# Kernel optimization log

Hardware: AMD Instinct MI355X
Metric: run time of the kernel (lower is better)

Reference implementation:

```python
import jax, jax.numpy as jnp
import numpy as np

NEG_SLOPE = 0.2  # keras 'leaky_relu' default negative slope

def _leaky_relu(t):
    return jnp.where(t >= 0, t, NEG_SLOPE * t)

def setup_inputs() -> dict:
    key = jax.random.key(0)
    kx, kq, kk, kv, ko, kg = jax.random.split(key, 6)
    B, H, W, C, A = 4, 64, 64, 256, 128
    x = jax.random.normal(kx, (B, H, W, C), dtype=jnp.float32)
    # 1x1 conv kernels == [Cin, Cout] matrices; glorot-normal-ish scaling
    Wq = jax.random.normal(kq, (C, A), dtype=jnp.float32) * (2.0 / (C + A)) ** 0.5
    Wk = jax.random.normal(kk, (C, A), dtype=jnp.float32) * (2.0 / (C + A)) ** 0.5
    Wv = jax.random.normal(kv, (C, A), dtype=jnp.float32) * (2.0 / (C + A)) ** 0.5
    Wo = jax.random.normal(ko, (A, C), dtype=jnp.float32) * (2.0 / (A + C)) ** 0.5
    # ChannelLearnableMultiplier weight: truncated_normal(0, 0.01) ~ small values near 0
    w_gamma = jax.random.normal(kg, (1, 1, 1, C), dtype=jnp.float32) * 0.01
    return {"x": x, "Wq": Wq, "Wk": Wk, "Wv": Wv, "Wo": Wo, "w_gamma": w_gamma}

def reference(x, Wq, Wk, Wv, Wo, w_gamma):
    B, H, W, C = x.shape
    A = Wq.shape[1]
    # 1x1 conv projections with leaky_relu activation, flatten spatial -> [B, N, A]
    q = _leaky_relu(jnp.einsum('bhwc,ca->bhwa', x, Wq)).reshape(B, H * W, A)
    k = _leaky_relu(jnp.einsum('bhwc,ca->bhwa', x, Wk)).reshape(B, H * W, A)
    v = _leaky_relu(jnp.einsum('bhwc,ca->bhwa', x, Wv)).reshape(B, H * W, A)
    # keras Attention(use_scale=False, score_mode='dot'): softmax(q k^T) v
    scores = jnp.einsum('bnd,bmd->bnm', q, k)          # [B, N, N]
    attn = jax.nn.softmax(scores, axis=-1)
    o = jnp.einsum('bnm,bmd->bnd', attn, v)            # [B, N, A]
    o = o.reshape(B, H, W, A)
    # output 1x1 conv, linear activation
    y = jnp.einsum('bhwa,ac->bhwc', o, Wo)
    # ChannelLearnableMultiplier: tanh(relu(1 + w)) * y
    return jnp.tanh(jax.nn.relu(1.0 + w_gamma)) * y
```

## Files before the change

kernel.cpp:

```cpp
#include <hip/hip_runtime.h>
#include <hip/hip_bf16.h>
#include <cstdint>
#include <cstddef>

typedef __bf16 bf16x8 __attribute__((ext_vector_type(8)));
typedef _Float16 f16x8 __attribute__((ext_vector_type(8)));
typedef short short8 __attribute__((ext_vector_type(8)));
typedef short short4v __attribute__((ext_vector_type(4)));
typedef float f32x4 __attribute__((ext_vector_type(4)));

#if defined(__HIP_DEVICE_COMPILE__)
  #define MFMA16BF(a,b,c)  __builtin_amdgcn_mfma_f32_16x16x16bf16_1k((a),(b),(c),0,0,0)
  #define MFMA32F16(a,b,c) __builtin_amdgcn_mfma_f32_16x16x32_f16((a),(b),(c),0,0,0)
  #define MFMA32BF(a,b,c)  __builtin_amdgcn_mfma_f32_16x16x32_bf16((a),(b),(c),0,0,0)
#else
  #define MFMA16BF(a,b,c)  (c)
  #define MFMA32F16(a,b,c) (c)
  #define MFMA32BF(a,b,c)  (c)
#endif

#if defined(__HIP_DEVICE_COMPILE__) && __has_builtin(__builtin_amdgcn_exp2f)
  #define EXP2F(x) __builtin_amdgcn_exp2f(x)
#else
  #define EXP2F(x) exp2f(x)
#endif

__device__ __forceinline__ void barrier_lds_only() {
    asm volatile("s_waitcnt lgkmcnt(0)\n\ts_barrier" ::: "memory");
}

__device__ __forceinline__ unsigned short f2bf(float f) {
    union { float f; uint32_t u; } v; v.f = f;
    uint32_t u = v.u;
    return (unsigned short)((u + 0x7FFFu + ((u >> 16) & 1u)) >> 16);
}
__device__ __forceinline__ float bf2f(unsigned short h) {
    union { uint32_t u; float f; } v; v.u = ((uint32_t)h) << 16;
    return v.f;
}
__device__ __forceinline__ unsigned short f2h(float f) {
    union { _Float16 h; unsigned short u; } v; v.h = (_Float16)f;
    return v.u;
}

__global__ __launch_bounds__(256) void qkv_kernel(
    const float* __restrict__ x,
    const float* __restrict__ Wq,
    const float* __restrict__ Wk,
    const float* __restrict__ Wv,
    unsigned short* __restrict__ qkv_ws)
{
    const int rowtile = blockIdx.x;
    const int proj    = blockIdx.y;
    const float* W = (proj == 0) ? Wq : ((proj == 1) ? Wk : Wv);
    unsigned short* outqk = qkv_ws + (size_t)proj * 2097152u;
    unsigned short* vt    = qkv_ws + (size_t)2 * 2097152u;
    const bool need_lo = (proj < 2);

    const int tid  = threadIdx.x;
    const int lane = tid & 63, wave = tid >> 6;
    const int lo   = lane & 15, quad = lane >> 4;

    __shared__ __align__(16) unsigned short Xh[64][72], Xl[64][72];
    __shared__ __align__(16) unsigned short Wh[128][72], Wl[128][72];

    f32x4 acc[8];
    #pragma unroll
    for (int i = 0; i < 8; ++i) acc[i] = (f32x4){0.f, 0.f, 0.f, 0.f};

    for (int kc = 0; kc < 4; ++kc) {
        __syncthreads();
        #pragma unroll
        for (int i = 0; i < 4; ++i) {
            int flat4 = (i * 256 + tid) * 4;
            int row = flat4 >> 6, col = flat4 & 63;
            float4 tv4 = *(const float4*)(x + (size_t)(rowtile * 64 + row) * 256 + kc * 64 + col);
            float tv[4] = {tv4.x, tv4.y, tv4.z, tv4.w};
            short4v h, l;
            #pragma unroll
            for (int j = 0; j < 4; ++j) {
                unsigned short hj = f2bf(tv[j]);
                h[j] = (short)hj;
                l[j] = (short)f2bf(tv[j] - bf2f(hj));
            }
            *(short4v*)(&Xh[row][col]) = h;
            if (need_lo) *(short4v*)(&Xl[row][col]) = l;
        }
        {
            int n = tid & 127;
            for (int g = (tid >> 7); g < 16; g += 2) {
                int k0 = g * 4;
                short4v h, l;
                #pragma unroll
                for (int j = 0; j < 4; ++j) {
                    float wv = W[(size_t)(kc * 64 + k0 + j) * 128 + n];
                    unsigned short hj = f2bf(wv);
                    h[j] = (short)hj;
                    l[j] = (short)f2bf(wv - bf2f(hj));
                }
                *(short4v*)(&Wh[n][k0]) = h;
                if (need_lo) *(short4v*)(&Wl[n][k0]) = l;
            }
        }
        __syncthreads();
        #pragma unroll
        for (int ks = 0; ks < 2; ++ks) {
            bf16x8 ah = *(const bf16x8*)(&Xh[wave * 16 + lo][ks * 32 + quad * 8]);
            #pragma unroll
            for (int nb = 0; nb < 8; ++nb) {
                bf16x8 bh = *(const bf16x8*)(&Wh[nb * 16 + lo][ks * 32 + quad * 8]);
                acc[nb] = MFMA32BF(ah, bh, acc[nb]);
                if (need_lo) {
                    bf16x8 al = *(const bf16x8*)(&Xl[wave * 16 + lo][ks * 32 + quad * 8]);
                    bf16x8 bl = *(const bf16x8*)(&Wl[nb * 16 + lo][ks * 32 + quad * 8]);
                    acc[nb] = MFMA32BF(al, bh, acc[nb]);
                    acc[nb] = MFMA32BF(ah, bl, acc[nb]);
                }
            }
        }
    }
    if (proj < 2) {
        #pragma unroll
        for (int nb = 0; nb < 8; ++nb) {
            #pragma unroll
            for (int r = 0; r < 4; ++r) {
                float v = acc[nb][r];
                v = (v >= 0.f) ? v : 0.2f * v;
                int m = rowtile * 64 + wave * 16 + quad * 4 + r;
                outqk[(size_t)m * 128 + nb * 16 + lo] = f2h(v);
            }
        }
    } else {
        const int b  = rowtile >> 6;
        const int sb = (rowtile & 63) * 64;
        #pragma unroll
        for (int nb = 0; nb < 8; ++nb) {
            #pragma unroll
            for (int r = 0; r < 4; ++r) {
                float v = acc[nb][r];
                v = (v >= 0.f) ? v : 0.2f * v;
                int seq = sb + wave * 16 + quad * 4 + r;
                int d   = nb * 16 + lo;
                vt[(size_t)b * 524288 + (size_t)d * 4096 + seq] = f2bf(v);
            }
        }
    }
}

__global__ __launch_bounds__(256) void attn_kernel(
    const unsigned short* __restrict__ qkv_ws,
    unsigned short* __restrict__ part,
    float* __restrict__ lpart,
    int chunk)
{
    const int b  = blockIdx.x;
    const int qt = blockIdx.y;
    const int z  = blockIdx.z;
    const int tid  = threadIdx.x;
    const int lane = tid & 63, wave = tid >> 6;
    const int lo   = lane & 15, quad = lane >> 4;

    const unsigned short* q  = qkv_ws;
    const unsigned short* k  = qkv_ws + 2097152u;
    const unsigned short* vt = qkv_ws + (size_t)2 * 2097152u + (size_t)b * 524288u;

    __shared__ __align__(16) unsigned short Ks[2][32][136];
    __shared__ __align__(16) unsigned short Vt[2][128][40];

    const int qbase = qt * 128 + wave * 32;
    f16x8 qf[2][4];
    #pragma unroll
    for (int g = 0; g < 2; ++g)
        #pragma unroll
        for (int ks = 0; ks < 4; ++ks)
            qf[g][ks] = *(const f16x8*)(q + ((size_t)(b * 4096 + qbase + g * 16 + lo)) * 128
                                          + ks * 32 + quad * 8);

    f32x4 oacc[2][8];
    #pragma unroll
    for (int g = 0; g < 2; ++g)
        #pragma unroll
        for (int i = 0; i < 8; ++i) oacc[g][i] = (f32x4){0.f, 0.f, 0.f, 0.f};
    float Lsum[2] = {1e-30f, 1e-30f};

    const float LOG2E  = 1.44269504088896f;
    const float NSHIFT = -40.0f * 1.44269504088896f;

    const int krow0 = tid >> 4, kcol0 = (tid & 15) * 8;
    const int krow1 = 16 + (tid >> 4);
    const int vd = tid >> 2, vc = tid & 3;
    const int vst  = vc >> 1;
    const int colA = ((2 * vc) & 3) * 8 + vst * 4;
    const int colB = ((2 * vc + 1) & 3) * 8 + vst * 4;

    const int niter = chunk >> 5;
    const int sbase = z * chunk;

    short8 ka, kb, va, vb;
    ka = *(const short8*)(k + ((size_t)(b * 4096 + sbase + krow0)) * 128 + kcol0);
    kb = *(const short8*)(k + ((size_t)(b * 4096 + sbase + krow1)) * 128 + kcol0);
    va = *(const short8*)(vt + (size_t)vd * 4096 + sbase + vc * 8);
    vb = *(const short8*)(vt + (size_t)(vd + 64) * 4096 + sbase + vc * 8);
    *(short8*)(&Ks[0][krow0][kcol0]) = ka;
    *(short8*)(&Ks[0][krow1][kcol0]) = kb;
    {
        short4v a0 = {va[0], va[1], va[2], va[3]}, a1 = {va[4], va[5], va[6], va[7]};
        short4v b0 = {vb[0], vb[1], vb[2], vb[3]}, b1 = {vb[4], vb[5], vb[6], vb[7]};
        *(short4v*)(&Vt[0][vd][colA])      = a0;
        *(short4v*)(&Vt[0][vd][colB])      = a1;
        *(short4v*)(&Vt[0][vd + 64][colA]) = b0;
        *(short4v*)(&Vt[0][vd + 64][colB]) = b1;
    }
    if (1 < niter) {
        const int s1 = sbase + 32;
        ka = *(const short8*)(k + ((size_t)(b * 4096 + s1 + krow0)) * 128 + kcol0);
        kb = *(const short8*)(k + ((size_t)(b * 4096 + s1 + krow1)) * 128 + kcol0);
        va = *(const short8*)(vt + (size_t)vd * 4096 + s1 + vc * 8);
        vb = *(const short8*)(vt + (size_t)(vd + 64) * 4096 + s1 + vc * 8);
    }
    barrier_lds_only();

    short4v Pp[2][2];

    for (int kt = 0; kt < niter; ++kt) {
        const int cur = kt & 1, oth = cur ^ 1;

        f32x4 sT[2][2];
        sT[0][0] = (f32x4){0.f,0.f,0.f,0.f}; sT[0][1] = (f32x4){0.f,0.f,0.f,0.f};
        sT[1][0] = (f32x4){0.f,0.f,0.f,0.f}; sT[1][1] = (f32x4){0.f,0.f,0.f,0.f};
        #pragma unroll
        for (int ks = 0; ks < 4; ++ks) {
            #pragma unroll
            for (int st = 0; st < 2; ++st) {
                f16x8 kf = *(const f16x8*)(&Ks[cur][st * 16 + lo][ks * 32 + quad * 8]);
                sT[0][st] = MFMA32F16(kf, qf[0][ks], sT[0][st]);
                sT[1][st] = MFMA32F16(kf, qf[1][ks], sT[1][st]);
            }
        }
        if (kt > 0) {
            #pragma unroll
            for (int nb = 0; nb < 8; ++nb) {
                short8 vv = *(const short8*)(&Vt[oth][nb * 16 + lo][quad * 8]);
                short4v v0 = {vv[0], vv[1], vv[2], vv[3]};
                short4v v1 = {vv[4], vv[5], vv[6], vv[7]};
                #pragma unroll
                for (int g = 0; g < 2; ++g) {
                    oacc[g][nb] = MFMA16BF(Pp[g][0], v0, oacc[g][nb]);
                    oacc[g][nb] = MFMA16BF(Pp[g][1], v1, oacc[g][nb]);
                }
            }
        }
        barrier_lds_only();
        if (kt + 1 < niter) {
            *(short8*)(&Ks[oth][krow0][kcol0]) = ka;
            *(short8*)(&Ks[oth][krow1][kcol0]) = kb;
            short4v a0 = {va[0], va[1], va[2], va[3]}, a1 = {va[4], va[5], va[6], va[7]};
            short4v b0 = {vb[0], vb[1], vb[2], vb[3]}, b1 = {vb[4], vb[5], vb[6], vb[7]};
            *(short4v*)(&Vt[oth][vd][colA])      = a0;
            *(short4v*)(&Vt[oth][vd][colB])      = a1;
            *(short4v*)(&Vt[oth][vd + 64][colA]) = b0;
            *(short4v*)(&Vt[oth][vd + 64][colB]) = b1;
        }
        if (kt + 2 < niter) {
            const int s2 = sbase + (kt + 2) * 32;
            ka = *(const short8*)(k + ((size_t)(b * 4096 + s2 + krow0)) * 128 + kcol0);
            kb = *(const short8*)(k + ((size_t)(b * 4096 + s2 + krow1)) * 128 + kcol0);
            va = *(const short8*)(vt + (size_t)vd * 4096 + s2 + vc * 8);
            vb = *(const short8*)(vt + (size_t)(vd + 64) * 4096 + s2 + vc * 8);
        }
        #pragma unroll
        for (int g = 0; g < 2; ++g) {
            #pragma unroll
            for (int st = 0; st < 2; ++st) {
                #pragma unroll
                for (int r = 0; r < 4; ++r) {
                    float t = fminf(fmaf(sT[g][st][r], LOG2E, NSHIFT), 125.0f);
                    union { float f; uint32_t u; } pv; pv.f = EXP2F(t);
                    unsigned short pt = (unsigned short)(pv.u >> 16);
                    Lsum[g] += bf2f(pt);
                    Pp[g][st][r] = (short)pt;
                }
            }
        }
        barrier_lds_only();
    }
    {
        const int last = (niter - 1) & 1;
        #pragma unroll
        for (int nb = 0; nb < 8; ++nb) {
            short8 vv = *(const short8*)(&Vt[last][nb * 16 + lo][quad * 8]);
            short4v v0 = {vv[0], vv[1], vv[2], vv[3]};
            short4v v1 = {vv[4], vv[5], vv[6], vv[7]};
            #pragma unroll
            for (int g = 0; g < 2; ++g) {
                oacc[g][nb] = MFMA16BF(Pp[g][0], v0, oacc[g][nb]);
                oacc[g][nb] = MFMA16BF(Pp[g][1], v1, oacc[g][nb]);
            }
        }
    }

    #pragma unroll
    for (int g = 0; g < 2; ++g) {
        float xr = Lsum[g];
        xr += __shfl_xor(xr, 16, 64);
        xr += __shfl_xor(xr, 32, 64);
        Lsum[g] = xr;
    }
    #pragma unroll
    for (int g = 0; g < 2; ++g) {
        #pragma unroll
        for (int nb = 0; nb < 8; ++nb) {
            #pragma unroll
            for (int r = 0; r < 4; ++r) {
                int m = b * 4096 + qbase + g * 16 + quad * 4 + r;
                part[((size_t)z * 16384 + m) * 128 + nb * 16 + lo] = f2bf(oacc[g][nb][r]);
            }
        }
        if (lane < 16) {
            int m = b * 4096 + qbase + g * 16 + lane;
            lpart[(size_t)z * 16384 + m] = Lsum[g];
        }
    }
}

__global__ __launch_bounds__(256) void outproj_kernel(
    const unsigned short* __restrict__ part,
    const float* __restrict__ lpart,
    const float* __restrict__ Wo,
    const float* __restrict__ wg,
    float* __restrict__ out,
    int nsplit)
{
    const int rowtile = blockIdx.x;
    const int tid  = threadIdx.x;
    const int lane = tid & 63, wave = tid >> 6;
    const int lo   = lane & 15, quad = lane >> 4;

    __shared__ __align__(16) unsigned short Os[32][136];
    __shared__ __align__(16) unsigned short WoT[128][136];
    __shared__ float gl[256];

    {
        float g = 1.0f + wg[tid];
        if (g < 0.f) g = 0.f;
        gl[tid] = tanhf(g);
    }
    #pragma unroll
    for (int i = 0; i < 2; ++i) {
        int flat = (i * 256 + tid) * 8;
        int row = flat >> 7, col = flat & 127;
        int m = rowtile * 32 + row;
        float acc8[8] = {0.f,0.f,0.f,0.f,0.f,0.f,0.f,0.f};
        float l = 0.f;
        for (int zz = 0; zz < nsplit; ++zz) {
            short8 t = *(const short8*)(part + ((size_t)zz * 16384 + m) * 128 + col);
            #pragma unroll
            for (int j = 0; j < 8; ++j) acc8[j] += bf2f((unsigned short)t[j]);
            l += lpart[(size_t)zz * 16384 + m];
        }
        float inv = 1.0f / l;
        short8 o8;
        #pragma unroll
        for (int j = 0; j < 8; ++j) o8[j] = (short)f2bf(acc8[j] * inv);
        *(short8*)(&Os[row][col]) = o8;
    }

    const int rg = wave & 1, csub = wave >> 1;

    for (int ch = 0; ch < 2; ++ch) {
        if (ch) __syncthreads();
        {
            int c = tid & 127;
            for (int g = (tid >> 7); g < 16; g += 2) {
                int a0 = g * 8;
                short8 t;
                #pragma unroll
                for (int j = 0; j < 8; ++j)
                    t[j] = (short)f2bf(Wo[(size_t)(a0 + j) * 256 + ch * 128 + c]);
                *(short8*)(&WoT[c][a0]) = t;
            }
        }
        __syncthreads();

        f32x4 acc[4];
        #pragma unroll
        for (int i = 0; i < 4; ++i) acc[i] = (f32x4){0.f, 0.f, 0.f, 0.f};
        #pragma unroll
        for (int ks = 0; ks < 4; ++ks) {
            bf16x8 a = *(const bf16x8*)(&Os[rg * 16 + lo][ks * 32 + quad * 8]);
            #pragma unroll
            for (int nb = 0; nb < 4; ++nb) {
                bf16x8 bf = *(const bf16x8*)(&WoT[csub * 64 + nb * 16 + lo][ks * 32 + quad * 8]);
                acc[nb] = MFMA32BF(a, bf, acc[nb]);
            }
        }
        #pragma unroll
        for (int nb = 0; nb < 4; ++nb) {
            int c = ch * 128 + csub * 64 + nb * 16 + lo;
            float g = gl[c];
            #pragma unroll
            for (int r = 0; r < 4; ++r) {
                int m = rowtile * 32 + rg * 16 + quad * 4 + r;
                out[(size_t)m * 256 + c] = acc[nb][r] * g;
            }
        }
    }
}

extern "C" void kernel_launch(void* const* d_in, const int* in_sizes, int n_in,
                              void* d_out, int out_size, void* d_ws, size_t ws_size,
                              hipStream_t stream) {
    const float* x  = (const float*)d_in[0];
    const float* Wq = (const float*)d_in[1];
    const float* Wk = (const float*)d_in[2];
    const float* Wv = (const float*)d_in[3];
    const float* Wo = (const float*)d_in[4];
    const float* wg = (const float*)d_in[5];
    float* out = (float*)d_out;

    unsigned short* ws = (unsigned short*)d_ws;
    const int nsplit = (ws_size >= (size_t)47000000) ? 8 : 4;
    const int chunk  = 4096 / nsplit;

    unsigned short* qkv_ws = ws;
    unsigned short* part   = ws + (size_t)3 * 2097152u;
    float* lpart = (float*)(part + (size_t)nsplit * 2097152u);

    qkv_kernel<<<dim3(256, 3), 256, 0, stream>>>(x, Wq, Wk, Wv, qkv_ws);
    attn_kernel<<<dim3(4, 32, nsplit), 256, 0, stream>>>(qkv_ws, part, lpart, chunk);
    outproj_kernel<<<dim3(512), 256, 0, stream>>>(part, lpart, Wo, wg, out, nsplit);
}
```

Measured before the change: 180.3 us.

## Pre-split weights into MFMA fragment layout and fuse QKV projections per tile

Adds a small prep kernel that converts Wq/Wk/Wv once into bf16 hi/lo pairs in MFMA fragment order, transposes Wo to bf16, and computes the gamma multiplier. The QKV kernel then handles all three projections in one block per row tile, reading weight fragments straight from global memory, and double-buffers the x tile in LDS with register prefetch. Together these avoid converting the same weights in every block and converting x three times. The cost is an extra launch, more accumulator registers (three sets of eight) that may lower occupancy, and weight fragments read from global or L2 on each k-step instead of from LDS. The prep buffers reuse the partial-output workspace region, which is safe only because attention overwrites it after qkv has finished reading.

```diff
diff --git a/kernel.cpp b/kernel.cpp
--- a/kernel.cpp
+++ b/kernel.cpp
@@ -43,101 +43,176 @@
     return v.u;
 }
 
+__global__ __launch_bounds__(256) void prep_kernel(
+    const float* __restrict__ Wq, const float* __restrict__ Wk,
+    const float* __restrict__ Wv, const float* __restrict__ Wo,
+    const float* __restrict__ wg,
+    unsigned short* __restrict__ wfh,
+    unsigned short* __restrict__ wfl,
+    unsigned short* __restrict__ wot,
+    float* __restrict__ gamma)
+{
+    const int bid = blockIdx.x, t = threadIdx.x;
+    __shared__ __align__(16) unsigned short Tsc[64][136];
+    if (bid < 12) {
+        const int proj = bid >> 2, kc = bid & 3;
+        const float* W = (proj == 0) ? Wq : ((proj == 1) ? Wk : Wv);
+        #pragma unroll
+        for (int s = 0; s < 4; ++s) {
+            int idx = s * 256 + t;
+            int frag = idx >> 6, lane = idx & 63;
+            int ks = frag >> 3, nb = frag & 7;
+            int lo = lane & 15, quad = lane >> 4;
+            short8 h8, l8;
+            #pragma unroll
+            for (int j = 0; j < 8; ++j) {
+                float w = W[(size_t)(kc * 64 + ks * 32 + quad * 8 + j) * 128 + nb * 16 + lo];
+                unsigned short hi = f2bf(w);
+                h8[j] = (short)hi;
+                l8[j] = (short)f2bf(w - bf2f(hi));
+            }
+            size_t base = ((size_t)(proj * 4 + kc) * 16 + frag) * 512 + lane * 8;
+            *(short8*)(wfh + base) = h8;
+            if (proj < 2)
+                *(short8*)(wfl + base) = l8;
+        }
+    } else if (bid < 16) {
+        const int c0 = (bid - 12) * 64;
+        for (int r = 0; r < 32; ++r) {
+            int idx = r * 256 + t;
+            int a = idx >> 6, cc = idx & 63;
+            Tsc[cc][a] = f2bf(Wo[(size_t)a * 256 + c0 + cc]);
+        }
+        __syncthreads();
+        int cc = t >> 2, a0 = (t & 3) * 32;
+        #pragma unroll
+        for (int j = 0; j < 4; ++j)
+            *(short8*)(wot + (size_t)(c0 + cc) * 128 + a0 + j * 8) =
+                *(const short8*)(&Tsc[cc][a0 + j * 8]);
+    } else {
+        float g = 1.0f + wg[t];
+        if (g < 0.f) g = 0.f;
+        gamma[t] = tanhf(g);
+    }
+}
+
 __global__ __launch_bounds__(256) void qkv_kernel(
     const float* __restrict__ x,
-    const float* __restrict__ Wq,
-    const float* __restrict__ Wk,
-    const float* __restrict__ Wv,
+    const unsigned short* __restrict__ wfh,
+    const unsigned short* __restrict__ wfl,
     unsigned short* __restrict__ qkv_ws)
 {
     const int rowtile = blockIdx.x;
-    const int proj    = blockIdx.y;
-    const float* W = (proj == 0) ? Wq : ((proj == 1) ? Wk : Wv);
-    unsigned short* outqk = qkv_ws + (size_t)proj * 2097152u;
-    unsigned short* vt    = qkv_ws + (size_t)2 * 2097152u;
-    const bool need_lo = (proj < 2);
-
     const int tid  = threadIdx.x;
     const int lane = tid & 63, wave = tid >> 6;
     const int lo   = lane & 15, quad = lane >> 4;
 
-    __shared__ __align__(16) unsigned short Xh[64][72], Xl[64][72];
-    __shared__ __align__(16) unsigned short Wh[128][72], Wl[128][72];
-
-    f32x4 acc[8];
-    #pragma unroll
-    for (int i = 0; i < 8; ++i) acc[i] = (f32x4){0.f, 0.f, 0.f, 0.f};
+    __shared__ __align__(16) unsigned short Xh[2][64][72], Xl[2][64][72];
+
+    f32x4 acc[3][8];
+    #pragma unroll
+    for (int p = 0; p < 3; ++p)
+        #pragma unroll
+        for (int i = 0; i < 8; ++i) acc[p][i] = (f32x4){0.f, 0.f, 0.f, 0.f};
+
+    int xrow[4], xcol[4];
+    #pragma unroll
+    for (int i = 0; i < 4; ++i) {
+        int flat4 = (i * 256 + tid) * 4;
+        xrow[i] = flat4 >> 6;
+        xcol[i] = flat4 & 63;
+    }
+    const float* xb = x + (size_t)rowtile * 64 * 256;
+
+    #pragma unroll
+    for (int i = 0; i < 4; ++i) {
+        float4 tv4 = *(const float4*)(xb + (size_t)xrow[i] * 256 + 0 * 64 + xcol[i]);
+        float tv[4] = {tv4.x, tv4.y, tv4.z, tv4.w};
+        short4v h, l;
+        #pragma unroll
+        for (int j = 0; j < 4; ++j) {
+            unsigned short hj = f2bf(tv[j]);
+            h[j] = (short)hj;
+            l[j] = (short)f2bf(tv[j] - bf2f(hj));
+        }
+        *(short4v*)(&Xh[0][xrow[i]][xcol[i]]) = h;
+        *(short4v*)(&Xl[0][xrow[i]][xcol[i]]) = l;
+    }
+    float4 xr[4];
+    #pragma unroll
+    for (int i = 0; i < 4; ++i)
+        xr[i] = *(const float4*)(xb + (size_t)xrow[i] * 256 + 1 * 64 + xcol[i]);
+    barrier_lds_only();
 
     for (int kc = 0; kc < 4; ++kc) {
-        __syncthreads();
-        #pragma unroll
-        for (int i = 0; i < 4; ++i) {
-            int flat4 = (i * 256 + tid) * 4;
-            int row = flat4 >> 6, col = flat4 & 63;
-            float4 tv4 = *(const float4*)(x + (size_t)(rowtile * 64 + row) * 256 + kc * 64 + col);
-            float tv[4] = {tv4.x, tv4.y, tv4.z, tv4.w};
-            short4v h, l;
-            #pragma unroll
-            for (int j = 0; j < 4; ++j) {
-                unsigned short hj = f2bf(tv[j]);
-                h[j] = (short)hj;
-                l[j] = (short)f2bf(tv[j] - bf2f(hj));
-            }
-            *(short4v*)(&Xh[row][col]) = h;
-            if (need_lo) *(short4v*)(&Xl[row][col]) = l;
-        }
-        {
-            int n = tid & 127;
-            for (int g = (tid >> 7); g < 16; g += 2) {
-                int k0 = g * 4;
+        const int cur = kc & 1, oth = cur ^ 1;
+        #pragma unroll
+        for (int proj = 0; proj < 3; ++proj) {
+            const unsigned short* wh = wfh + ((size_t)(proj * 4 + kc) * 16) * 512 + lane * 8;
+            const unsigned short* wl = wfl + ((size_t)(proj * 4 + kc) * 16) * 512 + lane * 8;
+            #pragma unroll
+            for (int ks = 0; ks < 2; ++ks) {
+                bf16x8 ah = *(const bf16x8*)(&Xh[cur][wave * 16 + lo][ks * 32 + quad * 8]);
+                bf16x8 al = *(const bf16x8*)(&Xl[cur][wave * 16 + lo][ks * 32 + quad * 8]);
+                #pragma unroll
+                for (int nb = 0; nb < 8; ++nb) {
+                    bf16x8 bh = *(const bf16x8*)(wh + (size_t)(ks * 8 + nb) * 512);
+                    acc[proj][nb] = MFMA32BF(ah, bh, acc[proj][nb]);
+                    if (proj < 2) {
+                        bf16x8 bl = *(const bf16x8*)(wl + (size_t)(ks * 8 + nb) * 512);
+                        acc[proj][nb] = MFMA32BF(al, bh, acc[proj][nb]);
+                        acc[proj][nb] = MFMA32BF(ah, bl, acc[proj][nb]);
+                    }
+                }
+            }
+        }
+        barrier_lds_only();
+        if (kc + 1 < 4) {
+            #pragma unroll
+            for (int i = 0; i < 4; ++i) {
+                float tv[4] = {xr[i].x, xr[i].y, xr[i].z, xr[i].w};
                 short4v h, l;
                 #pragma unroll
                 for (int j = 0; j < 4; ++j) {
-                    float wv = W[(size_t)(kc * 64 + k0 + j) * 128 + n];
-                    unsigned short hj = f2bf(wv);
+                    unsigned short hj = f2bf(tv[j]);
                     h[j] = (short)hj;
-                    l[j] = (short)f2bf(wv - bf2f(hj));
+                    l[j] = (short)f2bf(tv[j] - bf2f(hj));
                 }
-                *(short4v*)(&Wh[n][k0]) = h;
-                if (need_lo) *(short4v*)(&Wl[n][k0]) = l;
-            }
-        }
-        __syncthreads();
-        #pragma unroll
-        for (int ks = 0; ks < 2; ++ks) {
-            bf16x8 ah = *(const bf16x8*)(&Xh[wave * 16 + lo][ks * 32 + quad * 8]);
-            #pragma unroll
-            for (int nb = 0; nb < 8; ++nb) {
-                bf16x8 bh = *(const bf16x8*)(&Wh[nb * 16 + lo][ks * 32 + quad * 8]);
-                acc[nb] = MFMA32BF(ah, bh, acc[nb]);
-                if (need_lo) {
-                    bf16x8 al = *(const bf16x8*)(&Xl[wave * 16 + lo][ks * 32 + quad * 8]);
-                    bf16x8 bl = *(const bf16x8*)(&Wl[nb * 16 + lo][ks * 32 + quad * 8]);
-                    acc[nb] = MFMA32BF(al, bh, acc[nb]);
-                    acc[nb] = MFMA32BF(ah, bl, acc[nb]);
-                }
-            }
-        }
-    }
-    if (proj < 2) {
+                *(short4v*)(&Xh[oth][xrow[i]][xcol[i]]) = h;
+                *(short4v*)(&Xl[oth][xrow[i]][xcol[i]]) = l;
+            }
+        }
+        if (kc + 2 < 4) {
+            #pragma unroll
+            for (int i = 0; i < 4; ++i)
+                xr[i] = *(const float4*)(xb + (size_t)xrow[i] * 256 + (kc + 2) * 64 + xcol[i]);
+        }
+        barrier_lds_only();
+    }
+
+    #pragma unroll
+    for (int p = 0; p < 2; ++p) {
+        unsigned short* outqk = qkv_ws + (size_t)p * 2097152u;
         #pragma unroll
         for (int nb = 0; nb < 8; ++nb) {
             #pragma unroll
             for (int r = 0; r < 4; ++r) {
-                float v = acc[nb][r];
+                float v = acc[p][nb][r];
                 v = (v >= 0.f) ? v : 0.2f * v;
                 int m = rowtile * 64 + wave * 16 + quad * 4 + r;
                 outqk[(size_t)m * 128 + nb * 16 + lo] = f2h(v);
             }
         }
-    } else {
+    }
+    {
+        unsigned short* vt = qkv_ws + (size_t)2 * 2097152u;
         const int b  = rowtile >> 6;
         const int sb = (rowtile & 63) * 64;
         #pragma unroll
         for (int nb = 0; nb < 8; ++nb) {
             #pragma unroll
             for (int r = 0; r < 4; ++r) {
-                float v = acc[nb][r];
+                float v = acc[2][nb][r];
                 v = (v >= 0.f) ? v : 0.2f * v;
                 int seq = sb + wave * 16 + quad * 4 + r;
                 int d   = nb * 16 + lo;
@@ -326,8 +401,8 @@
 __global__ __launch_bounds__(256) void outproj_kernel(
     const unsigned short* __restrict__ part,
     const float* __restrict__ lpart,
-    const float* __restrict__ Wo,
-    const float* __restrict__ wg,
+    const unsigned short* __restrict__ wot,
+    const float* __restrict__ gamma,
     float* __restrict__ out,
     int nsplit)
 {
@@ -338,13 +413,7 @@
 
     __shared__ __align__(16) unsigned short Os[32][136];
     __shared__ __align__(16) unsigned short WoT[128][136];
-    __shared__ float gl[256];
-
-    {
-        float g = 1.0f + wg[tid];
-        if (g < 0.f) g = 0.f;
-        gl[tid] = tanhf(g);
-    }
+
     #pragma unroll
     for (int i = 0; i < 2; ++i) {
         int flat = (i * 256 + tid) * 8;
@@ -366,20 +435,14 @@
     }
 
     const int rg = wave & 1, csub = wave >> 1;
+    const int wc = tid >> 1, wa0 = (tid & 1) * 64;
 
     for (int ch = 0; ch < 2; ++ch) {
         if (ch) __syncthreads();
-        {
-            int c = tid & 127;
-            for (int g = (tid >> 7); g < 16; g += 2) {
-                int a0 = g * 8;
-                short8 t;
-                #pragma unroll
-                for (int j = 0; j < 8; ++j)
-                    t[j] = (short)f2bf(Wo[(size_t)(a0 + j) * 256 + ch * 128 + c]);
-                *(short8*)(&WoT[c][a0]) = t;
-            }
-        }
+        #pragma unroll
+        for (int j = 0; j < 8; ++j)
+            *(short8*)(&WoT[wc][wa0 + j * 8]) =
+                *(const short8*)(wot + (size_t)(ch * 128 + wc) * 128 + wa0 + j * 8);
         __syncthreads();
 
         f32x4 acc[4];
@@ -397,7 +460,7 @@
         #pragma unroll
         for (int nb = 0; nb < 4; ++nb) {
             int c = ch * 128 + csub * 64 + nb * 16 + lo;
-            float g = gl[c];
+            float g = gamma[c];
             #pragma unroll
             for (int r = 0; r < 4; ++r) {
                 int m = rowtile * 32 + rg * 16 + quad * 4 + r;
@@ -424,9 +487,14 @@
 
     unsigned short* qkv_ws = ws;
     unsigned short* part   = ws + (size_t)3 * 2097152u;
+    unsigned short* wfh    = part;
+    unsigned short* wfl    = part + 98304u;
     float* lpart = (float*)(part + (size_t)nsplit * 2097152u);
-
-    qkv_kernel<<<dim3(256, 3), 256, 0, stream>>>(x, Wq, Wk, Wv, qkv_ws);
+    unsigned short* wot = (unsigned short*)(lpart + (size_t)nsplit * 16384u);
+    float* gamma = (float*)(wot + 32768u);
+
+    prep_kernel<<<dim3(17), 256, 0, stream>>>(Wq, Wk, Wv, Wo, wg, wfh, wfl, wot, gamma);
+    qkv_kernel<<<dim3(256), 256, 0, stream>>>(x, wfh, wfl, qkv_ws);
     attn_kernel<<<dim3(4, 32, nsplit), 256, 0, stream>>>(qkv_ws, part, lpart, chunk);
-    outproj_kernel<<<dim3(512), 256, 0, stream>>>(part, lpart, Wo, wg, out, nsplit);
-}
+    outproj_kernel<<<dim3(512), 256, 0, stream>>>(part, lpart, wot, gamma, out, nsplit);
+}
```

Result: faster. 175.7 us (-2.6%).
